# Kernel tuning notes

Measured on AMD Instinct MI355X. Metric: run time of the kernel, lower is better.

Reference implementation:

```python
import jax, jax.numpy as jnp
import numpy as np

D_MODEL = 1024
NUM_HEADS = 16
HEAD_DIM = D_MODEL // NUM_HEADS
B, S = 2, 2048


def setup_inputs() -> dict:
    key = jax.random.key(0)
    ks = jax.random.split(key, 6)
    scale = 0.02
    return {
        "x": jax.random.normal(ks[0], (B, S, D_MODEL), dtype=jnp.float32),
        "mask": jax.random.normal(ks[1], (S, S), dtype=jnp.float32),
        "Wqkv": jax.random.normal(ks[2], (D_MODEL, 3 * D_MODEL), dtype=jnp.float32) * scale,
        "bqkv": jax.random.normal(ks[3], (3 * D_MODEL,), dtype=jnp.float32) * scale,
        "Wout": jax.random.normal(ks[4], (D_MODEL, D_MODEL), dtype=jnp.float32) * scale,
        "bout": jax.random.normal(ks[5], (D_MODEL,), dtype=jnp.float32) * scale,
    }


def reference(x, mask, Wqkv, bqkv, Wout, bout):
    b, s, d = x.shape
    h, hd = NUM_HEADS, HEAD_DIM
    qkv = x @ Wqkv + bqkv                              # [b, s, 3d]
    qkv = qkv.reshape(b, s, h, 3 * hd).transpose(0, 2, 1, 3)  # [b, h, s, 3hd]
    q, k, v = jnp.split(qkv, 3, axis=-1)               # each [b, h, s, hd]
    scaled = jnp.einsum("bhqd,bhkd->bhqk", q, k) / jnp.sqrt(jnp.float32(hd))
    scaled = scaled + mask                             # mask [s, s] broadcasts
    attn = jax.nn.softmax(scaled, axis=-1)
    values = jnp.einsum("bhqk,bhkd->bhqd", attn, v)    # [b, h, s, hd]
    values = values.transpose(0, 2, 1, 3).reshape(b, s, d)
    return values @ Wout + bout
```

## Files before the change

kernel.cpp:

```cpp
#include <hip/hip_runtime.h>
#include <hip/hip_bf16.h>

#define D_MODEL 1024
#define NH 16
#define HD 64
#define BATCH 2
#define SEQ 2048
#define M_TOTAL (BATCH*SEQ)

typedef _Float16 f16;
typedef _Float16 half8 __attribute__((ext_vector_type(8)));
typedef _Float16 half4v __attribute__((ext_vector_type(4)));
typedef float floatx4 __attribute__((ext_vector_type(4)));

#if __has_builtin(__builtin_amdgcn_exp2f)
#define EXP2(x) __builtin_amdgcn_exp2f(x)
#else
#define EXP2(x) __expf(0.6931471805599453f * (x))
#endif

__device__ inline void gload_lds16(const void* g, void* l) {
    __builtin_amdgcn_global_load_lds(
        (const __attribute__((address_space(1))) unsigned int*)g,
        (__attribute__((address_space(3))) unsigned int*)l, 16, 0, 0);
}

__device__ void trans_body(const float* __restrict__ src, f16* __restrict__ dst,
                           int R, int C, int bx, int by) {
    __shared__ float tile[32][33];
    int tx = threadIdx.x & 31;
    int ty = threadIdx.x >> 5;
    int c0 = bx * 32;
    int r0 = by * 32;
    for (int yy = 0; yy < 32; yy += 8)
        tile[ty + yy][tx] = src[(long)(r0 + ty + yy) * C + c0 + tx];
    __syncthreads();
    for (int yy = 0; yy < 32; yy += 8)
        dst[(long)(c0 + ty + yy) * R + r0 + tx] = (f16)tile[tx][ty + yy];
}

__global__ __launch_bounds__(256) void prep(
    const float* __restrict__ x, f16* __restrict__ xh,
    const float* __restrict__ Wqkv, f16* __restrict__ WqkvT,
    const float* __restrict__ Wout, f16* __restrict__ WoutT)
{
    int bid = blockIdx.x;
    if (bid < 1024) {
        int i = bid * 256 + threadIdx.x;
        #pragma unroll
        for (int it = 0; it < 4; ++it, i += 262144) {
            float4 v = ((const float4*)x)[i];
            half4v o = { (f16)v.x, (f16)v.y, (f16)v.z, (f16)v.w };
            *(half4v*)(xh + (long)i * 4) = o;
        }
    } else if (bid < 1024 + 3072) {
        int t = bid - 1024;
        trans_body(Wqkv, WqkvT, 1024, 3072, t % 96, t / 96);
    } else {
        int t = bid - 4096;
        trans_body(Wout, WoutT, 1024, 1024, t % 32, t / 32);
    }
}

__global__ void l2scale_cvt(const float* __restrict__ src, f16* __restrict__ dst, int n4) {
    int i = blockIdx.x * blockDim.x + threadIdx.x;
    if (i < n4) {
        float4 v = ((const float4*)src)[i];
        const float L2E = 1.44269504f;
        half4v o = { (f16)(v.x * L2E), (f16)(v.y * L2E), (f16)(v.z * L2E), (f16)(v.w * L2E) };
        *(half4v*)(dst + (long)i * 4) = o;
    }
}

template<int MODE, int TN>
__global__ __launch_bounds__(256) void gemm_mfma(
    const f16* __restrict__ A, const f16* __restrict__ BT,
    const float* __restrict__ bias,
    f16* __restrict__ Qh, f16* __restrict__ Kh, f16* __restrict__ Vtg,
    float* __restrict__ out, int Kdim)
{
    constexpr int NF = TN / 32;
    __shared__ f16 Ah[128 * 64];
    __shared__ f16 Bh[TN * 64];
    int tid  = threadIdx.x;
    int wid  = tid >> 6;
    int lane = tid & 63;
    int quad = lane >> 4;
    int l16  = lane & 15;
    int m0 = blockIdx.y * 128;
    int n0 = blockIdx.x * TN;
    int mrow = (wid >> 1) * 64;
    int ncol = (wid & 1) * (TN / 2);
    int grow = lane >> 3;
    int gchunk = (lane & 7) ^ (grow & 7);
    int sw0 = ((quad)     ^ (l16 & 7)) * 8;
    int sw1 = ((quad + 4) ^ (l16 & 7)) * 8;

    floatx4 acc[4][NF];
    #pragma unroll
    for (int mb = 0; mb < 4; mb++)
        #pragma unroll
        for (int nb = 0; nb < NF; nb++) acc[mb][nb] = (floatx4){0.f, 0.f, 0.f, 0.f};

    const f16* Abase = A + (long)m0 * Kdim;
    const f16* Bbase = BT + (long)n0 * Kdim;

    for (int k0 = 0; k0 < Kdim; k0 += 64) {
        #pragma unroll
        for (int j = 0; j < 4; j++) {
            int r = j * 32 + wid * 8 + grow;
            gload_lds16(Abase + (long)r * Kdim + k0 + gchunk * 8, &Ah[(j * 32 + wid * 8) * 64]);
        }
        #pragma unroll
        for (int j = 0; j < TN / 32; j++) {
            int r = j * 32 + wid * 8 + grow;
            gload_lds16(Bbase + (long)r * Kdim + k0 + gchunk * 8, &Bh[(j * 32 + wid * 8) * 64]);
        }
        __syncthreads();
        #pragma unroll
        for (int h = 0; h < 2; h++) {
            int sw = h ? sw1 : sw0;
            half8 af[4];
            #pragma unroll
            for (int mb = 0; mb < 4; mb++)
                af[mb] = *(const half8*)&Ah[(mrow + mb * 16 + l16) * 64 + sw];
            #pragma unroll
            for (int nb = 0; nb < NF; nb++) {
                half8 bf = *(const half8*)&Bh[(ncol + nb * 16 + l16) * 64 + sw];
                #pragma unroll
                for (int mb = 0; mb < 4; mb++)
                    acc[mb][nb] = __builtin_amdgcn_mfma_f32_16x16x32_f16(af[mb], bf, acc[mb][nb], 0, 0, 0);
            }
        }
        __syncthreads();
    }

    #pragma unroll
    for (int nb = 0; nb < NF; nb++) {
        int n = n0 + ncol + nb * 16 + l16;
        float bv = bias[n];
        int head = 0, t = 0, d = 0;
        if (MODE == 0) { head = n / 192; int rem = n % 192; t = rem / 64; d = rem % 64; }
        #pragma unroll
        for (int mb = 0; mb < 4; mb++) {
            int mbase = m0 + mrow + mb * 16 + quad * 4;
            if (MODE == 0) {
                int b = mbase >> 11;
                int s = mbase & 2047;
                long bh = b * NH + head;
                if (t == 2) {
                    half4v pack;
                    #pragma unroll
                    for (int r = 0; r < 4; r++) pack[r] = (f16)(acc[mb][nb][r] + bv);
                    *(half4v*)&Vtg[(bh * HD + d) * SEQ + s] = pack;
                } else if (t == 0) {
                    #pragma unroll
                    for (int r = 0; r < 4; r++)
                        Qh[(bh * SEQ + s + r) * HD + d] = (f16)((acc[mb][nb][r] + bv) * 0.18033688f);
                } else {
                    #pragma unroll
                    for (int r = 0; r < 4; r++)
                        Kh[(bh * SEQ + s + r) * HD + d] = (f16)(acc[mb][nb][r] + bv);
                }
            } else {
                #pragma unroll
                for (int r = 0; r < 4; r++)
                    out[(long)(mbase + r) * D_MODEL + n] = acc[mb][nb][r] + bv;
            }
        }
    }
}

__global__ __launch_bounds__(512) void attn(
    const f16* __restrict__ Qh, const f16* __restrict__ Kh, const f16* __restrict__ Vtg,
    const f16* __restrict__ E, f16* __restrict__ valh)
{
    __shared__ f16 Kl[2][64 * 64];
    __shared__ f16 Vt[2][64 * 64];
    __shared__ f16 Pl[8][16 * 68];
    int tid  = threadIdx.x;
    int wid  = tid >> 6;
    int lane = tid & 63;
    int quad = lane >> 4;
    int l16  = lane & 15;

    int id   = blockIdx.y * 16 + blockIdx.x;
    int xcd  = id & 7;
    int slot = id >> 3;
    int bh   = ((xcd & 3) << 3) | (slot >> 3);
    int qx   = ((xcd >> 2) << 3) | (slot & 7);
    int b  = bh >> 4;
    int h  = bh & 15;
    int qblk = qx * 128;
    int q0 = qblk + wid * 16;

    int wrow = wid * 8 + (lane >> 3);
    int kchunk = (lane & 7) ^ (wrow & 7);
    int sw0 = ((quad)     ^ (l16 & 7)) * 8;
    int sw1 = ((quad + 4) ^ (l16 & 7)) * 8;

    const f16* Qbase = Qh + ((long)bh * SEQ + q0) * HD;
    half8 qf[2];
    #pragma unroll
    for (int c = 0; c < 2; c++)
        qf[c] = *(const half8*)&Qbase[(long)l16 * HD + c * 32 + quad * 8];

    half8 onesv;
    #pragma unroll
    for (int j = 0; j < 8; j++) onesv[j] = (f16)1.0f;

    floatx4 Of[4];
    floatx4 ssum = (floatx4){0.f, 0.f, 0.f, 0.f};
    #pragma unroll
    for (int nb = 0; nb < 4; nb++) Of[nb] = (floatx4){0.f, 0.f, 0.f, 0.f};

    const f16* Kb = Kh + (long)bh * SEQ * HD;
    const f16* Vb = Vtg + (long)bh * HD * SEQ;
    const f16* Eb = E + (long)qblk * SEQ;

    auto stage = [&](int buf, int k0) {
        gload_lds16(Kb + (long)(k0 + wrow) * HD + kchunk * 8, &Kl[buf][(wid * 8) * 64]);
        gload_lds16(Vb + (long)wrow * SEQ + k0 + kchunk * 8, &Vt[buf][(wid * 8) * 64]);
    };

    stage(0, 0);
    __syncthreads();

    auto iter = [&](const int buf, int k0) {
        bool notlast = (k0 + 64 < SEQ);
        if (notlast) stage(buf ^ 1, k0 + 64);

        f16 ef[4][4];
        #pragma unroll
        for (int r = 0; r < 4; r++) {
            const f16* Erow = Eb + (long)(wid * 16 + quad * 4 + r) * SEQ + k0 + l16;
            #pragma unroll
            for (int kb = 0; kb < 4; kb++) ef[r][kb] = Erow[kb * 16];
        }

        floatx4 sc[4];
        __builtin_amdgcn_s_setprio(1);
        #pragma unroll
        for (int kb = 0; kb < 4; kb++) {
            half8 kf0 = *(const half8*)&Kl[buf][(kb * 16 + l16) * 64 + sw0];
            half8 kf1 = *(const half8*)&Kl[buf][(kb * 16 + l16) * 64 + sw1];
            floatx4 s = (floatx4){0.f, 0.f, 0.f, 0.f};
            s = __builtin_amdgcn_mfma_f32_16x16x32_f16(qf[0], kf0, s, 0, 0, 0);
            s = __builtin_amdgcn_mfma_f32_16x16x32_f16(qf[1], kf1, s, 0, 0, 0);
            sc[kb] = s;
        }
        __builtin_amdgcn_s_setprio(0);

        #pragma unroll
        for (int kb = 0; kb < 4; kb++)
            #pragma unroll
            for (int r = 0; r < 4; r++) {
                float p = EXP2(sc[kb][r] + (float)ef[r][kb]);
                Pl[wid][(quad * 4 + r) * 68 + kb * 16 + l16] = (f16)p;
            }

        half8 pf0 = *(const half8*)&Pl[wid][l16 * 68 + quad * 8];
        half8 pf1 = *(const half8*)&Pl[wid][l16 * 68 + 32 + quad * 8];

        __builtin_amdgcn_s_setprio(1);
        ssum = __builtin_amdgcn_mfma_f32_16x16x32_f16(pf0, onesv, ssum, 0, 0, 0);
        ssum = __builtin_amdgcn_mfma_f32_16x16x32_f16(pf1, onesv, ssum, 0, 0, 0);
        #pragma unroll
        for (int nb = 0; nb < 4; nb++) {
            half8 vf0 = *(const half8*)&Vt[buf][(nb * 16 + l16) * 64 + sw0];
            half8 vf1 = *(const half8*)&Vt[buf][(nb * 16 + l16) * 64 + sw1];
            Of[nb] = __builtin_amdgcn_mfma_f32_16x16x32_f16(pf0, vf0, Of[nb], 0, 0, 0);
            Of[nb] = __builtin_amdgcn_mfma_f32_16x16x32_f16(pf1, vf1, Of[nb], 0, 0, 0);
        }
        __builtin_amdgcn_s_setprio(0);

        __syncthreads();
    };

    for (int k0 = 0; k0 < SEQ; k0 += 128) {
        iter(0, k0);
        iter(1, k0 + 64);
    }

    float rinv[4];
    #pragma unroll
    for (int r = 0; r < 4; r++) rinv[r] = 1.f / ssum[r];

    #pragma unroll
    for (int nb = 0; nb < 4; nb++)
        #pragma unroll
        for (int r = 0; r < 4; r++) {
            int q = q0 + quad * 4 + r;
            int d = nb * 16 + l16;
            valh[((long)(b * SEQ + q)) * D_MODEL + h * HD + d] = (f16)(Of[nb][r] * rinv[r]);
        }
}

extern "C" void kernel_launch(void* const* d_in, const int* in_sizes, int n_in,
                              void* d_out, int out_size, void* d_ws, size_t ws_size,
                              hipStream_t stream) {
    const float* x    = (const float*)d_in[0];
    const float* mask = (const float*)d_in[1];
    const float* Wqkv = (const float*)d_in[2];
    const float* bqkv = (const float*)d_in[3];
    const float* Wout = (const float*)d_in[4];
    const float* bout = (const float*)d_in[5];
    float* out = (float*)d_out;

    char* ws = (char*)d_ws;
    f16* xh    = (f16*)(ws + 0);
    f16* E     = (f16*)(ws + 0);
    f16* WqkvT = (f16*)(ws + 8388608);
    f16* WoutT = (f16*)(ws + 14680064);
    f16* Qh    = (f16*)(ws + 16777216);
    f16* Kh    = (f16*)(ws + 25165824);
    f16* Vtg   = (f16*)(ws + 33554432);
    f16* valh  = (f16*)(ws + 41943040);

    prep<<<5120, 256, 0, stream>>>(x, xh, Wqkv, WqkvT, Wout, WoutT);
    gemm_mfma<0, 128><<<dim3(24, 32), 256, 0, stream>>>(xh, WqkvT, bqkv, Qh, Kh, Vtg, nullptr, 1024);
    l2scale_cvt<<<4096, 256, 0, stream>>>(mask, E, SEQ * SEQ / 4);
    attn<<<dim3(16, 32), 512, 0, stream>>>(Qh, Kh, Vtg, E, valh);
    gemm_mfma<1, 64><<<dim3(16, 32), 256, 0, stream>>>(valh, WoutT, bout, nullptr, nullptr, nullptr, out, 1024);
}
```

Before: 216.9 us.

## Double-buffer GEMM LDS tiles and fold mask conversion into attention

The GEMM main loop switches from a single 64-wide K tile with two barriers per step to double-buffered 32-wide K tiles. The next tile is prefetched while the current one feeds the MFMAs, so global-to-LDS latency can overlap compute. The separate mask-to-fp16 conversion kernel is removed. The attention kernel now reads the fp32 mask directly and applies the log2(e) scale with an FMA, saving one launch and a 16MB write/read pass. In exchange, attention reads twice as many mask bytes per tile (re-read by all 32 batch-head blocks), and the GEMM runs twice as many loop iterations, each with half the MFMA work per barrier.

Measured after the change: 213.0 us. No clear change (-1.8%).

```diff
diff --git a/kernel.cpp b/kernel.cpp
--- a/kernel.cpp
+++ b/kernel.cpp
@@ -62,16 +62,6 @@
     }
 }
 
-__global__ void l2scale_cvt(const float* __restrict__ src, f16* __restrict__ dst, int n4) {
-    int i = blockIdx.x * blockDim.x + threadIdx.x;
-    if (i < n4) {
-        float4 v = ((const float4*)src)[i];
-        const float L2E = 1.44269504f;
-        half4v o = { (f16)(v.x * L2E), (f16)(v.y * L2E), (f16)(v.z * L2E), (f16)(v.w * L2E) };
-        *(half4v*)(dst + (long)i * 4) = o;
-    }
-}
-
 template<int MODE, int TN>
 __global__ __launch_bounds__(256) void gemm_mfma(
     const f16* __restrict__ A, const f16* __restrict__ BT,
@@ -80,8 +70,8 @@
     float* __restrict__ out, int Kdim)
 {
     constexpr int NF = TN / 32;
-    __shared__ f16 Ah[128 * 64];
-    __shared__ f16 Bh[TN * 64];
+    __shared__ f16 Ah[2][128 * 32];
+    __shared__ f16 Bh[2][TN * 32];
     int tid  = threadIdx.x;
     int wid  = tid >> 6;
     int lane = tid & 63;
@@ -91,10 +81,9 @@
     int n0 = blockIdx.x * TN;
     int mrow = (wid >> 1) * 64;
     int ncol = (wid & 1) * (TN / 2);
-    int grow = lane >> 3;
-    int gchunk = (lane & 7) ^ (grow & 7);
-    int sw0 = ((quad)     ^ (l16 & 7)) * 8;
-    int sw1 = ((quad + 4) ^ (l16 & 7)) * 8;
+    int srow = lane >> 2;
+    int gchunk = (lane & 3) ^ (srow & 3);
+    int sw = (quad ^ (l16 & 3)) * 8;
 
     floatx4 acc[4][NF];
     #pragma unroll
@@ -105,34 +94,42 @@
     const f16* Abase = A + (long)m0 * Kdim;
     const f16* Bbase = BT + (long)n0 * Kdim;
 
-    for (int k0 = 0; k0 < Kdim; k0 += 64) {
-        #pragma unroll
-        for (int j = 0; j < 4; j++) {
-            int r = j * 32 + wid * 8 + grow;
-            gload_lds16(Abase + (long)r * Kdim + k0 + gchunk * 8, &Ah[(j * 32 + wid * 8) * 64]);
-        }
-        #pragma unroll
-        for (int j = 0; j < TN / 32; j++) {
-            int r = j * 32 + wid * 8 + grow;
-            gload_lds16(Bbase + (long)r * Kdim + k0 + gchunk * 8, &Bh[(j * 32 + wid * 8) * 64]);
-        }
-        __syncthreads();
-        #pragma unroll
-        for (int h = 0; h < 2; h++) {
-            int sw = h ? sw1 : sw0;
-            half8 af[4];
+    auto stage = [&](int buf, int k0) {
+        #pragma unroll
+        for (int j = 0; j < 2; j++) {
+            int r = wid * 32 + j * 16 + srow;
+            gload_lds16(Abase + (long)r * Kdim + k0 + gchunk * 8, &Ah[buf][(wid * 32 + j * 16) * 32]);
+        }
+        if (TN == 128) {
+            #pragma unroll
+            for (int j = 0; j < 2; j++) {
+                int r = wid * 32 + j * 16 + srow;
+                gload_lds16(Bbase + (long)r * Kdim + k0 + gchunk * 8, &Bh[buf][(wid * 32 + j * 16) * 32]);
+            }
+        } else {
+            int r = wid * 16 + srow;
+            gload_lds16(Bbase + (long)r * Kdim + k0 + gchunk * 8, &Bh[buf][(wid * 16) * 32]);
+        }
+    };
+
+    stage(0, 0);
+    __syncthreads();
+    int cur = 0;
+    for (int k0 = 0; k0 < Kdim; k0 += 32) {
+        if (k0 + 32 < Kdim) stage(cur ^ 1, k0 + 32);
+        half8 af[4];
+        #pragma unroll
+        for (int mb = 0; mb < 4; mb++)
+            af[mb] = *(const half8*)&Ah[cur][(mrow + mb * 16 + l16) * 32 + sw];
+        #pragma unroll
+        for (int nb = 0; nb < NF; nb++) {
+            half8 bf = *(const half8*)&Bh[cur][(ncol + nb * 16 + l16) * 32 + sw];
             #pragma unroll
             for (int mb = 0; mb < 4; mb++)
-                af[mb] = *(const half8*)&Ah[(mrow + mb * 16 + l16) * 64 + sw];
-            #pragma unroll
-            for (int nb = 0; nb < NF; nb++) {
-                half8 bf = *(const half8*)&Bh[(ncol + nb * 16 + l16) * 64 + sw];
-                #pragma unroll
-                for (int mb = 0; mb < 4; mb++)
-                    acc[mb][nb] = __builtin_amdgcn_mfma_f32_16x16x32_f16(af[mb], bf, acc[mb][nb], 0, 0, 0);
-            }
+                acc[mb][nb] = __builtin_amdgcn_mfma_f32_16x16x32_f16(af[mb], bf, acc[mb][nb], 0, 0, 0);
         }
         __syncthreads();
+        cur ^= 1;
     }
 
     #pragma unroll
@@ -173,7 +170,7 @@
 
 __global__ __launch_bounds__(512) void attn(
     const f16* __restrict__ Qh, const f16* __restrict__ Kh, const f16* __restrict__ Vtg,
-    const f16* __restrict__ E, f16* __restrict__ valh)
+    const float* __restrict__ mask, f16* __restrict__ valh)
 {
     __shared__ f16 Kl[2][64 * 64];
     __shared__ f16 Vt[2][64 * 64];
@@ -216,7 +213,7 @@
 
     const f16* Kb = Kh + (long)bh * SEQ * HD;
     const f16* Vb = Vtg + (long)bh * HD * SEQ;
-    const f16* Eb = E + (long)qblk * SEQ;
+    const float* Mb = mask + (long)qblk * SEQ;
 
     auto stage = [&](int buf, int k0) {
         gload_lds16(Kb + (long)(k0 + wrow) * HD + kchunk * 8, &Kl[buf][(wid * 8) * 64]);
@@ -226,16 +223,18 @@
     stage(0, 0);
     __syncthreads();
 
+    const float L2E = 1.44269504f;
+
     auto iter = [&](const int buf, int k0) {
         bool notlast = (k0 + 64 < SEQ);
         if (notlast) stage(buf ^ 1, k0 + 64);
 
-        f16 ef[4][4];
+        float ef[4][4];
         #pragma unroll
         for (int r = 0; r < 4; r++) {
-            const f16* Erow = Eb + (long)(wid * 16 + quad * 4 + r) * SEQ + k0 + l16;
+            const float* Mrow = Mb + (long)(wid * 16 + quad * 4 + r) * SEQ + k0 + l16;
             #pragma unroll
-            for (int kb = 0; kb < 4; kb++) ef[r][kb] = Erow[kb * 16];
+            for (int kb = 0; kb < 4; kb++) ef[r][kb] = Mrow[kb * 16];
         }
 
         floatx4 sc[4];
@@ -255,7 +254,7 @@
         for (int kb = 0; kb < 4; kb++)
             #pragma unroll
             for (int r = 0; r < 4; r++) {
-                float p = EXP2(sc[kb][r] + (float)ef[r][kb]);
+                float p = EXP2(__builtin_fmaf(ef[r][kb], L2E, sc[kb][r]));
                 Pl[wid][(quad * 4 + r) * 68 + kb * 16 + l16] = (f16)p;
             }
 
@@ -309,7 +308,6 @@
 
     char* ws = (char*)d_ws;
     f16* xh    = (f16*)(ws + 0);
-    f16* E     = (f16*)(ws + 0);
     f16* WqkvT = (f16*)(ws + 8388608);
     f16* WoutT = (f16*)(ws + 14680064);
     f16* Qh    = (f16*)(ws + 16777216);
@@ -319,7 +317,6 @@
 
     prep<<<5120, 256, 0, stream>>>(x, xh, Wqkv, WqkvT, Wout, WoutT);
     gemm_mfma<0, 128><<<dim3(24, 32), 256, 0, stream>>>(xh, WqkvT, bqkv, Qh, Kh, Vtg, nullptr, 1024);
-    l2scale_cvt<<<4096, 256, 0, stream>>>(mask, E, SEQ * SEQ / 4);
-    attn<<<dim3(16, 32), 512, 0, stream>>>(Qh, Kh, Vtg, E, valh);
+    attn<<<dim3(16, 32), 512, 0, stream>>>(Qh, Kh, Vtg, mask, valh);
     gemm_mfma<1, 64><<<dim3(16, 32), 256, 0, stream>>>(valh, WoutT, bout, nullptr, nullptr, nullptr, out, 1024);
 }
```
